# Kernel tuning notes

Measured on AMD Instinct MI355X. Metric: run time of the kernel, lower is better.

## Reference

```python
import jax, jax.numpy as jnp
import numpy as np

THETA = 1.2
XI = 0.3


def setup_inputs() -> dict:
    key = jax.random.key(0)
    k1, k2 = jax.random.split(key)
    B, D = 8192, 512
    x = jax.random.normal(k1, (B, D), dtype=jnp.float32)
    y = jax.random.randint(k2, (B,), 0, 1000, dtype=jnp.int64)
    return {"x": x, "y": y}


def reference(x, y):
    B = x.shape[0]
    # per-sample L2 normalization: n_i = x_i / ||x_i||
    n = x / jnp.linalg.norm(x, axis=1, keepdims=True)  # [B, D]
    # pairwise squared distances ||n_i - n_j||^2 = |n_i|^2 + |n_j|^2 - 2 n_i.n_j
    sq = jnp.sum(n * n, axis=1)                        # [B]
    G = n @ n.T                                        # [B, B]
    dist2 = sq[:, None] + sq[None, :] - 2.0 * G        # [B, B]
    # indicator: +1 if same label else -1 (symmetric)
    ind = jnp.where(y[:, None] == y[None, :], 1.0, -1.0)
    # original loops i in [0,B), j in [i,B): upper triangle including diagonal
    idx = jnp.arange(B)
    mask = (idx[None, :] >= idx[:, None]).astype(x.dtype)
    hinge = jnp.maximum(THETA - dist2, 0.0)
    total = jnp.sum(mask * (XI + ind * hinge))
    m_scalar = 1.0 / (B * B - B)
    return m_scalar * total
```

## Files before the change

kernel.cpp:

```cpp
#include <hip/hip_runtime.h>
#include <cstdint>
#include <cstddef>

#define THETA 1.2f
#define XI 0.3f
#define BDIM 8192
#define DDIM 512
#define NTILE 64
#define NUPPER 2080
#define GRID 1024
#define NPAIRS_UP (((double)BDIM * (double)(BDIM + 1)) * 0.5)

typedef float f32x4 __attribute__((ext_vector_type(4)));
typedef int i32x8 __attribute__((ext_vector_type(8)));


__global__ __launch_bounds__(256) void normalize_rows(
    const float* __restrict__ x, unsigned char* __restrict__ nf8,
    float* __restrict__ sq, unsigned int* __restrict__ counter)
{
    if (blockIdx.x == 0 && threadIdx.x == 0) { *counter = 0u; }
    int row = blockIdx.x * 4 + (threadIdx.x >> 6);
    int l = threadIdx.x & 63;
    const float4* xr = (const float4*)(x + (size_t)row * DDIM);
    float4 f0 = xr[l];
    float4 f1 = xr[l + 64];
    float s = f0.x*f0.x + f0.y*f0.y + f0.z*f0.z + f0.w*f0.w
            + f1.x*f1.x + f1.y*f1.y + f1.z*f1.z + f1.w*f1.w;
    #pragma unroll
    for (int m = 1; m < 64; m <<= 1) s += __shfl_xor(s, m);
    float rn = rsqrtf(s);
    int pk0 = __builtin_amdgcn_cvt_pk_fp8_f32(f0.x * rn, f0.y * rn, 0, false);
    pk0     = __builtin_amdgcn_cvt_pk_fp8_f32(f0.z * rn, f0.w * rn, pk0, true);
    int pk1 = __builtin_amdgcn_cvt_pk_fp8_f32(f1.x * rn, f1.y * rn, 0, false);
    pk1     = __builtin_amdgcn_cvt_pk_fp8_f32(f1.z * rn, f1.w * rn, pk1, true);
    size_t base = (size_t)(row >> 4) * 4 * 2048;
    int within = ((row & 15) + ((l >> 3) & 3) * 16) * 32 + (l & 7) * 4;
    int kc0 = l >> 5;
    int kc1 = (l >> 5) + 2;
    *(int*)(nf8 + base + (size_t)kc0 * 2048 + within) = pk0;
    *(int*)(nf8 + base + (size_t)kc1 * 2048 + within) = pk1;
    if (l == 0) sq[row] = s * rn * rn;
}

__device__ __forceinline__ void decode_tile(int u, int& ti, int& tj) {
    int t = (int)((sqrtf(8.0f * (float)u + 1.0f) - 1.0f) * 0.5f);
    while ((t + 1) * (t + 2) / 2 <= u) ++t;
    while (t * (t + 1) / 2 > u) --t;
    tj = t;
    ti = u - t * (t + 1) / 2;
}

__global__ __launch_bounds__(256, 3) void gram_hinge(
    const unsigned char* __restrict__ nf8, const float* __restrict__ sq,
    const int* __restrict__ y, double* __restrict__ part,
    unsigned int* __restrict__ counter, float* __restrict__ out)
{
    __shared__ unsigned char As[2][16384];
    __shared__ float wpart[4];
    __shared__ double dpart[4];
    __shared__ int is_last;

    int tid = threadIdx.x;
    int w = tid >> 6, l = tid & 63;
    int wr = w >> 1, wc = w & 1;
    int lr = l & 15, q = l >> 4;

    auto stageA = [&](unsigned char* dAb, int pti, int pc) {
        #pragma unroll
        for (int i = 0; i < 4; ++i) {
            int t = w * 4 + i;
            int rf = t >> 1, half = t & 1;
            const unsigned char* src = nf8
                + ((size_t)((pti * 8 + rf) * 4 + pc)) * 2048 + half * 1024 + l * 16;
            __builtin_amdgcn_global_load_lds(
                (const __attribute__((address_space(1))) void*)src,
                (__attribute__((address_space(3))) void*)(dAb + t * 1024), 16, 0, 0);
        }
    };

    float acc0 = 0.f, acc1 = 0.f, acc2 = 0.f, acc3 = 0.f;

    int u = blockIdx.x;
    int ti, tj;
    decode_tile(u, ti, tj);

    stageA(As[0], ti, 0);

    while (u < NUPPER) {
        int u_next = u + GRID;
        bool have_next = (u_next < NUPPER);
        int ti_n = 0, tj_n = 0;
        if (have_next) decode_tile(u_next, ti_n, tj_n);

        f32x4 accv[4][4] = {};

        #pragma unroll 1
        for (int c = 0; c < 4; ++c) {
            i32x8 bf[4];
            #pragma unroll
            for (int ni = 0; ni < 4; ++ni)
                bf[ni] = *(const i32x8*)(nf8
                    + ((size_t)((tj * 8 + wc * 4 + ni) * 4 + c)) * 2048 + l * 32);
            __builtin_amdgcn_sched_barrier(0);

            if (c < 3) {
                stageA(As[(c + 1) & 1], ti, c + 1);
                asm volatile("s_waitcnt vmcnt(12)" ::: "memory");
            } else if (have_next) {
                stageA(As[0], ti_n, 0);
                asm volatile("s_waitcnt vmcnt(12)" ::: "memory");
            } else {
                asm volatile("s_waitcnt vmcnt(8)" ::: "memory");
            }
            asm volatile("s_barrier" ::: "memory");

            const unsigned char* Ab = As[c & 1];
            __builtin_amdgcn_s_setprio(1);
            #pragma unroll
            for (int mi = 0; mi < 4; ++mi) {
                i32x8 af = *(const i32x8*)(Ab + (wr * 4 + mi) * 2048 + l * 32);
                #pragma unroll
                for (int ni = 0; ni < 4; ++ni)
                    accv[mi][ni] = __builtin_amdgcn_mfma_scale_f32_16x16x128_f8f6f4(
                        af, bf[ni], accv[mi][ni],
                        0, 0, 0, 0x7F7F7F7F, 0, 0x7F7F7F7F);
            }
            __builtin_amdgcn_s_setprio(0);

            asm volatile("s_barrier" ::: "memory");
        }

        {
            int jb = tj * 128 + wc * 64 + lr;
            float sqj[4]; int yj[4];
            #pragma unroll
            for (int ni = 0; ni < 4; ++ni) {
                sqj[ni] = sq[jb + ni * 16];
                yj[ni]  = y[jb + ni * 16];
            }
            bool skip = (ti == tj) && (wr > wc);
            bool full = (ti != tj) || (wc > wr);
            if (!skip) {
                if (full) {
                    #pragma unroll
                    for (int mi = 0; mi < 4; ++mi) {
                        #pragma unroll
                        for (int r = 0; r < 4; ++r) {
                            int ia = ti * 128 + wr * 64 + mi * 16 + q * 4 + r;
                            float ci = THETA - sq[ia];
                            int yi = y[ia];
                            float h0 = fmaxf(fmaf(2.f, accv[mi][0][r], ci - sqj[0]), 0.f);
                            acc0 += (yi == yj[0]) ? h0 : -h0;
                            float h1 = fmaxf(fmaf(2.f, accv[mi][1][r], ci - sqj[1]), 0.f);
                            acc1 += (yi == yj[1]) ? h1 : -h1;
                            float h2 = fmaxf(fmaf(2.f, accv[mi][2][r], ci - sqj[2]), 0.f);
                            acc2 += (yi == yj[2]) ? h2 : -h2;
                            float h3 = fmaxf(fmaf(2.f, accv[mi][3][r], ci - sqj[3]), 0.f);
                            acc3 += (yi == yj[3]) ? h3 : -h3;
                        }
                    }
                } else {
                    #pragma unroll
                    for (int mi = 0; mi < 4; ++mi) {
                        #pragma unroll
                        for (int r = 0; r < 4; ++r) {
                            int rl_ = mi * 16 + q * 4 + r;
                            int ia = ti * 128 + wr * 64 + rl_;
                            float ci = THETA - sq[ia];
                            int yi = y[ia];
                            #pragma unroll
                            for (int ni = 0; ni < 4; ++ni) {
                                float h = fmaxf(fmaf(2.f, accv[mi][ni][r], ci - sqj[ni]), 0.f);
                                float sh = (yi == yj[ni]) ? h : -h;
                                if (ni * 16 + lr >= rl_) acc0 += sh;
                            }
                        }
                    }
                }
            }
        }

        u = u_next; ti = ti_n; tj = tj_n;
    }

    float local = (acc0 + acc1) + (acc2 + acc3);
    #pragma unroll
    for (int off = 32; off > 0; off >>= 1) local += __shfl_down(local, off);
    if (l == 0) wpart[w] = local;
    __syncthreads();
    if (tid == 0) {
        double ssum = (double)wpart[0] + (double)wpart[1]
                    + (double)wpart[2] + (double)wpart[3];
        __hip_atomic_store(&part[blockIdx.x], ssum, __ATOMIC_RELEASE, __HIP_MEMORY_SCOPE_AGENT);
        unsigned int ticket = __hip_atomic_fetch_add(
            counter, 1u, __ATOMIC_ACQ_REL, __HIP_MEMORY_SCOPE_AGENT);
        is_last = (ticket == GRID - 1) ? 1 : 0;
    }
    __syncthreads();
    if (is_last) {
        double s = 0.0;
        for (int i = tid; i < GRID; i += 256)
            s += __hip_atomic_load(&part[i], __ATOMIC_ACQUIRE, __HIP_MEMORY_SCOPE_AGENT);
        #pragma unroll
        for (int off = 32; off > 0; off >>= 1) s += __shfl_down(s, off);
        if (l == 0) dpart[w] = s;
        __syncthreads();
        if (tid == 0) {
            double total = (dpart[0] + dpart[1] + dpart[2] + dpart[3])
                         + (double)XI * NPAIRS_UP;
            const double m = 1.0 / ((double)BDIM * (double)BDIM - (double)BDIM);
            out[0] = (float)(total * m);
        }
    }
}

extern "C" void kernel_launch(void* const* d_in, const int* in_sizes, int n_in,
                              void* d_out, int out_size, void* d_ws, size_t ws_size,
                              hipStream_t stream) {
    const float* x = (const float*)d_in[0];
    const int* y = (const int*)d_in[1];
    float* out = (float*)d_out;

    unsigned char* nf8 = (unsigned char*)d_ws;
    char* p = (char*)d_ws + (size_t)BDIM * DDIM;
    float* sq = (float*)p;
    unsigned int* counter = (unsigned int*)(p + (size_t)BDIM * 4);
    double* part = (double*)(p + (size_t)BDIM * 4 + 64);

    normalize_rows<<<BDIM / 4, 256, 0, stream>>>(x, nf8, sq, counter);
    gram_hinge<<<GRID, 256, 0, stream>>>(nf8, sq, y, part, counter, out);
}
```

Baseline: 120.4 us.

## Load A and B fragments directly to registers with even/odd double buffering

Drops the LDS staging of A tiles, together with their barriers and waitcnt management. Each wave now loads its A and B fp8 fragments straight from global memory into registers, ping-ponging between even and odd K-chunk register sets so the next chunk's loads overlap the current MFMAs. The grid is halved and the occupancy hint lowered to 2 blocks per CU to make room for the larger register footprint. The cost is that A rows shared between the two column-waves are now fetched from global/L2 twice instead of once through LDS, and fewer blocks cover the 2080 tiles.

```diff
diff --git a/kernel.cpp b/kernel.cpp
--- a/kernel.cpp
+++ b/kernel.cpp
@@ -8,7 +8,7 @@
 #define DDIM 512
 #define NTILE 64
 #define NUPPER 2080
-#define GRID 1024
+#define GRID 512
 #define NPAIRS_UP (((double)BDIM * (double)(BDIM + 1)) * 0.5)
 
 typedef float f32x4 __attribute__((ext_vector_type(4)));
@@ -51,12 +51,11 @@
     ti = u - t * (t + 1) / 2;
 }
 
-__global__ __launch_bounds__(256, 3) void gram_hinge(
+__global__ __launch_bounds__(256, 2) void gram_hinge(
     const unsigned char* __restrict__ nf8, const float* __restrict__ sq,
     const int* __restrict__ y, double* __restrict__ part,
     unsigned int* __restrict__ counter, float* __restrict__ out)
 {
-    __shared__ unsigned char As[2][16384];
     __shared__ float wpart[4];
     __shared__ double dpart[4];
     __shared__ int is_last;
@@ -66,69 +65,62 @@
     int wr = w >> 1, wc = w & 1;
     int lr = l & 15, q = l >> 4;
 
-    auto stageA = [&](unsigned char* dAb, int pti, int pc) {
-        #pragma unroll
-        for (int i = 0; i < 4; ++i) {
-            int t = w * 4 + i;
-            int rf = t >> 1, half = t & 1;
-            const unsigned char* src = nf8
-                + ((size_t)((pti * 8 + rf) * 4 + pc)) * 2048 + half * 1024 + l * 16;
-            __builtin_amdgcn_global_load_lds(
-                (const __attribute__((address_space(1))) void*)src,
-                (__attribute__((address_space(3))) void*)(dAb + t * 1024), 16, 0, 0);
-        }
-    };
-
     float acc0 = 0.f, acc1 = 0.f, acc2 = 0.f, acc3 = 0.f;
 
     int u = blockIdx.x;
     int ti, tj;
     decode_tile(u, ti, tj);
 
-    stageA(As[0], ti, 0);
-
     while (u < NUPPER) {
-        int u_next = u + GRID;
-        bool have_next = (u_next < NUPPER);
-        int ti_n = 0, tj_n = 0;
-        if (have_next) decode_tile(u_next, ti_n, tj_n);
+        const unsigned char* pA = nf8 + ((size_t)((ti * 8 + wr * 4) * 4)) * 2048 + l * 32;
+        const unsigned char* pB = nf8 + ((size_t)((tj * 8 + wc * 4) * 4)) * 2048 + l * 32;
 
         f32x4 accv[4][4] = {};
+        i32x8 afe[4], bfe[4], afo[4], bfo[4];
+
+        #pragma unroll
+        for (int f = 0; f < 4; ++f) {
+            afe[f] = *(const i32x8*)(pA + f * 8192);
+            bfe[f] = *(const i32x8*)(pB + f * 8192);
+        }
 
         #pragma unroll 1
-        for (int c = 0; c < 4; ++c) {
-            i32x8 bf[4];
-            #pragma unroll
-            for (int ni = 0; ni < 4; ++ni)
-                bf[ni] = *(const i32x8*)(nf8
-                    + ((size_t)((tj * 8 + wc * 4 + ni) * 4 + c)) * 2048 + l * 32);
-            __builtin_amdgcn_sched_barrier(0);
-
-            if (c < 3) {
-                stageA(As[(c + 1) & 1], ti, c + 1);
-                asm volatile("s_waitcnt vmcnt(12)" ::: "memory");
-            } else if (have_next) {
-                stageA(As[0], ti_n, 0);
-                asm volatile("s_waitcnt vmcnt(12)" ::: "memory");
-            } else {
-                asm volatile("s_waitcnt vmcnt(8)" ::: "memory");
-            }
-            asm volatile("s_barrier" ::: "memory");
-
-            const unsigned char* Ab = As[c & 1];
+        for (int cc = 0; cc < 2; ++cc) {
+            int codd = cc * 2 + 1;
+            #pragma unroll
+            for (int f = 0; f < 4; ++f) {
+                afo[f] = *(const i32x8*)(pA + f * 8192 + codd * 2048);
+                bfo[f] = *(const i32x8*)(pB + f * 8192 + codd * 2048);
+            }
+            __builtin_amdgcn_sched_barrier(0);
             __builtin_amdgcn_s_setprio(1);
             #pragma unroll
-            for (int mi = 0; mi < 4; ++mi) {
-                i32x8 af = *(const i32x8*)(Ab + (wr * 4 + mi) * 2048 + l * 32);
+            for (int mi = 0; mi < 4; ++mi)
                 #pragma unroll
                 for (int ni = 0; ni < 4; ++ni)
                     accv[mi][ni] = __builtin_amdgcn_mfma_scale_f32_16x16x128_f8f6f4(
-                        af, bf[ni], accv[mi][ni],
+                        afe[mi], bfe[ni], accv[mi][ni],
                         0, 0, 0, 0x7F7F7F7F, 0, 0x7F7F7F7F);
-            }
             __builtin_amdgcn_s_setprio(0);
-
-            asm volatile("s_barrier" ::: "memory");
+            __builtin_amdgcn_sched_barrier(0);
+            if (cc == 0) {
+                #pragma unroll
+                for (int f = 0; f < 4; ++f) {
+                    afe[f] = *(const i32x8*)(pA + f * 8192 + 2 * 2048);
+                    bfe[f] = *(const i32x8*)(pB + f * 8192 + 2 * 2048);
+                }
+            }
+            __builtin_amdgcn_sched_barrier(0);
+            __builtin_amdgcn_s_setprio(1);
+            #pragma unroll
+            for (int mi = 0; mi < 4; ++mi)
+                #pragma unroll
+                for (int ni = 0; ni < 4; ++ni)
+                    accv[mi][ni] = __builtin_amdgcn_mfma_scale_f32_16x16x128_f8f6f4(
+                        afo[mi], bfo[ni], accv[mi][ni],
+                        0, 0, 0, 0x7F7F7F7F, 0, 0x7F7F7F7F);
+            __builtin_amdgcn_s_setprio(0);
+            __builtin_amdgcn_sched_barrier(0);
         }
 
         {
@@ -181,7 +173,8 @@
             }
         }
 
-        u = u_next; ti = ti_n; tj = tj_n;
+        u += GRID;
+        if (u < NUPPER) decode_tile(u, ti, tj);
     }
 
     float local = (acc0 + acc1) + (acc2 + acc3);
```

Result: slower. 140.2 us (+16.4%).

## Double-buffer B fragments in registers and halve persistent grid

Applied to the files above, without the earlier changes.

B-operand register fragments are now prefetched one K-chunk ahead into alternating even/odd register sets, and the K loop is unrolled by two with fixed LDS buffers. The aim is to hide the global B-load latency behind the MFMA work, where before it sat on the critical path each chunk. To make room for the extra registers, occupancy drops from 3 to 2 blocks per CU and the persistent grid shrinks from 1024 to 512 blocks. Each block therefore handles more tiles, and the lower occupancy may hurt latency hiding.

```diff
diff --git a/kernel.cpp b/kernel.cpp
--- a/kernel.cpp
+++ b/kernel.cpp
@@ -8,7 +8,7 @@
 #define DDIM 512
 #define NTILE 64
 #define NUPPER 2080
-#define GRID 1024
+#define GRID 512
 #define NPAIRS_UP (((double)BDIM * (double)(BDIM + 1)) * 0.5)
 
 typedef float f32x4 __attribute__((ext_vector_type(4)));
@@ -51,7 +51,7 @@
     ti = u - t * (t + 1) / 2;
 }
 
-__global__ __launch_bounds__(256, 3) void gram_hinge(
+__global__ __launch_bounds__(256, 2) void gram_hinge(
     const unsigned char* __restrict__ nf8, const float* __restrict__ sq,
     const int* __restrict__ y, double* __restrict__ part,
     unsigned int* __restrict__ counter, float* __restrict__ out)
@@ -78,6 +78,12 @@
                 (__attribute__((address_space(3))) void*)(dAb + t * 1024), 16, 0, 0);
         }
     };
+    auto bload = [&](int ptj, int pc, i32x8* dst) {
+        #pragma unroll
+        for (int ni = 0; ni < 4; ++ni)
+            dst[ni] = *(const i32x8*)(nf8
+                + ((size_t)((ptj * 8 + wc * 4 + ni) * 4 + pc)) * 2048 + l * 32);
+    };
 
     float acc0 = 0.f, acc1 = 0.f, acc2 = 0.f, acc3 = 0.f;
 
@@ -85,6 +91,9 @@
     int ti, tj;
     decode_tile(u, ti, tj);
 
+    i32x8 bfe[4], bfo[4];
+
+    bload(tj, 0, bfe);
     stageA(As[0], ti, 0);
 
     while (u < NUPPER) {
@@ -96,38 +105,47 @@
         f32x4 accv[4][4] = {};
 
         #pragma unroll 1
-        for (int c = 0; c < 4; ++c) {
-            i32x8 bf[4];
-            #pragma unroll
-            for (int ni = 0; ni < 4; ++ni)
-                bf[ni] = *(const i32x8*)(nf8
-                    + ((size_t)((tj * 8 + wc * 4 + ni) * 4 + c)) * 2048 + l * 32);
-            __builtin_amdgcn_sched_barrier(0);
-
-            if (c < 3) {
-                stageA(As[(c + 1) & 1], ti, c + 1);
-                asm volatile("s_waitcnt vmcnt(12)" ::: "memory");
-            } else if (have_next) {
-                stageA(As[0], ti_n, 0);
-                asm volatile("s_waitcnt vmcnt(12)" ::: "memory");
-            } else {
-                asm volatile("s_waitcnt vmcnt(8)" ::: "memory");
-            }
-            asm volatile("s_barrier" ::: "memory");
-
-            const unsigned char* Ab = As[c & 1];
+        for (int cc = 0; cc < 2; ++cc) {
+            bload(tj, 2 * cc + 1, bfo);
+            stageA(As[1], ti, 2 * cc + 1);
+            asm volatile("s_waitcnt vmcnt(12)" ::: "memory");
+            asm volatile("s_barrier" ::: "memory");
             __builtin_amdgcn_s_setprio(1);
             #pragma unroll
             for (int mi = 0; mi < 4; ++mi) {
-                i32x8 af = *(const i32x8*)(Ab + (wr * 4 + mi) * 2048 + l * 32);
+                i32x8 af = *(const i32x8*)(As[0] + (wr * 4 + mi) * 2048 + l * 32);
                 #pragma unroll
                 for (int ni = 0; ni < 4; ++ni)
                     accv[mi][ni] = __builtin_amdgcn_mfma_scale_f32_16x16x128_f8f6f4(
-                        af, bf[ni], accv[mi][ni],
+                        af, bfe[ni], accv[mi][ni],
                         0, 0, 0, 0x7F7F7F7F, 0, 0x7F7F7F7F);
             }
             __builtin_amdgcn_s_setprio(0);
-
+            asm volatile("s_barrier" ::: "memory");
+
+            bool more = (cc == 0) || have_next;
+            int nti = (cc == 0) ? ti : ti_n;
+            int ntj = (cc == 0) ? tj : tj_n;
+            int nc  = (cc == 0) ? 2 : 0;
+            if (more) {
+                bload(ntj, nc, bfe);
+                stageA(As[0], nti, nc);
+                asm volatile("s_waitcnt vmcnt(12)" ::: "memory");
+            } else {
+                asm volatile("s_waitcnt vmcnt(0)" ::: "memory");
+            }
+            asm volatile("s_barrier" ::: "memory");
+            __builtin_amdgcn_s_setprio(1);
+            #pragma unroll
+            for (int mi = 0; mi < 4; ++mi) {
+                i32x8 af = *(const i32x8*)(As[1] + (wr * 4 + mi) * 2048 + l * 32);
+                #pragma unroll
+                for (int ni = 0; ni < 4; ++ni)
+                    accv[mi][ni] = __builtin_amdgcn_mfma_scale_f32_16x16x128_f8f6f4(
+                        af, bfo[ni], accv[mi][ni],
+                        0, 0, 0, 0x7F7F7F7F, 0, 0x7F7F7F7F);
+            }
+            __builtin_amdgcn_s_setprio(0);
             asm volatile("s_barrier" ::: "memory");
         }
 
```

Result: faster. 108.1 us (-10.2%).
